# Kernel tuning notes

Measured on AMD Instinct MI355X. Metric: run time of the kernel, lower is better.

## Reference

```python
import jax, jax.numpy as jnp
import numpy as np

BATCH = 4096
NUM_INPUTS = 784
WIDTH = 16000        # neurons per logic layer, divisible by NUM_CLASSES
N_HIDDEN = 4         # width->width layers stacked for scan (plus the input layer)
NUM_CLASSES = 10


def setup_inputs() -> dict:
    key = jax.random.key(0)
    ks = jax.random.split(key, 7)
    x = jax.random.bernoulli(ks[0], 0.5, (BATCH, NUM_INPUTS))
    idx_a0 = jax.random.randint(ks[1], (WIDTH,), 0, NUM_INPUTS, dtype=jnp.int32)
    idx_b0 = jax.random.randint(ks[2], (WIDTH,), 0, NUM_INPUTS, dtype=jnp.int32)
    neg0 = jax.random.bernoulli(ks[3], 0.5, (WIDTH, 2))
    idx_a = jax.random.randint(ks[4], (N_HIDDEN, WIDTH), 0, WIDTH, dtype=jnp.int32)
    idx_b = jax.random.randint(ks[5], (N_HIDDEN, WIDTH), 0, WIDTH, dtype=jnp.int32)
    neg = jax.random.bernoulli(ks[6], 0.5, (N_HIDDEN, WIDTH, 2))
    return {"x": x, "idx_a0": idx_a0, "idx_b0": idx_b0, "neg0": neg0,
            "idx_a": idx_a, "idx_b": idx_b, "neg": neg}


def _gate(a, b, nf):
    # gate = (maybe-NOT a) AND (maybe-NOT b); NOT on booleans == XOR with flag
    return (a ^ nf[:, 0]) & (b ^ nf[:, 1])


def reference(x, idx_a0, idx_b0, neg0, idx_a, idx_b, neg):
    # input layer: gather wires from the boolean input
    h = _gate(x[:, idx_a0], x[:, idx_b0], neg0)  # [BATCH, WIDTH] bool

    def step(h, p):
        ia, ib, nf = p
        return _gate(h[:, ia], h[:, ib], nf), None

    h, _ = jax.lax.scan(step, h, (idx_a, idx_b, neg))
    # GroupSum: popcount per class group -> int32 logits
    out = h.reshape(BATCH, NUM_CLASSES, WIDTH // NUM_CLASSES).sum(-1, dtype=jnp.int32)
    return out
```

## Files before the change

### kernel.cpp

```cpp
#include <hip/hip_runtime.h>


#define NIN   784
#define WIDTH 16000
#define NH    4
#define NC    10
#define GPC   1600
#define NBLK  128
#define TPB   1024
#define SSTR  13

typedef unsigned int u32;

__global__ void desc_kernel(const int* __restrict__ ia0, const int* __restrict__ ib0,
                            const int* __restrict__ n0,
                            const int* __restrict__ ia, const int* __restrict__ ib,
                            const int* __restrict__ n, u32* __restrict__ desc) {
    int t = blockIdx.x * blockDim.x + threadIdx.x;
    if (t >= (NH + 1) * WIDTH) return;
    int l = t / WIDTH, g = t % WIDTH;
    int a, b, na, nb;
    if (l == 0) { a = ia0[g]; b = ib0[g]; na = n0[2 * g]; nb = n0[2 * g + 1]; }
    else {
        int o = (l - 1) * WIDTH + g;
        a = ia[o]; b = ib[o]; na = n[2 * o]; nb = n[2 * o + 1];
    }
    desc[t] = (u32)a | ((u32)b << 14) | (na ? (1u << 28) : 0u) | (nb ? (1u << 29) : 0u);
}

__device__ __forceinline__ void gate(const u32* __restrict__ src, u32* __restrict__ dst,
                                     const u32* __restrict__ dp, int g) {
    u32 d  = dp[g];
    u32 a  = d & 0x3FFFu;
    u32 b  = (d >> 14) & 0x3FFFu;
    u32 ma = 0u - ((d >> 28) & 1u);
    u32 mb = 0u - ((d >> 29) & 1u);
    dst[g] = (src[a] ^ ma) & (src[b] ^ mb);
}

__launch_bounds__(TPB)
__global__ void net_kernel(const int* __restrict__ x, const u32* __restrict__ desc,
                           int* __restrict__ out) {
    __shared__ u32 xw[NIN];
    __shared__ u32 bufA[WIDTH];
    __shared__ u32 bufB[WIDTH];

    int w = blockIdx.x;
    int t = threadIdx.x;

    if (t < NIN) {
        const int* base = x + (size_t)(w * 32) * NIN + t;
        u32 acc = 0;
#pragma unroll
        for (int r = 0; r < 32; ++r)
            acc |= (base[(size_t)r * NIN] != 0 ? 1u : 0u) << r;
        xw[t] = acc;
    }
    __syncthreads();

    {
        const u32* dp = desc;
#pragma unroll 3
        for (int it = 0; it < 15; ++it) gate(xw, bufA, dp, t + it * TPB);
        if (t < WIDTH - 15 * TPB) gate(xw, bufA, dp, t + 15 * TPB);
    }

    u32* cur = bufA;
    u32* nxt = bufB;
    for (int l = 1; l <= NH; ++l) {
        __syncthreads();
        const u32* dp = desc + (size_t)l * WIDTH;
#pragma unroll 3
        for (int it = 0; it < 15; ++it) gate(cur, nxt, dp, t + it * TPB);
        if (t < WIDTH - 15 * TPB) gate(cur, nxt, dp, t + 15 * TPB);
        u32* tmp = cur; cur = nxt; nxt = tmp;
    }
    __syncthreads();

    u32* scratch = nxt;
    if (t < NC * 100) {
        int c = t / 100, j = t % 100;
        u32 p[12];
#pragma unroll
        for (int q = 0; q < 12; ++q) p[q] = 0;
#pragma unroll
        for (int k = 0; k < 16; ++k) {
            u32 carry = cur[c * GPC + k * 100 + j];
#pragma unroll
            for (int q = 0; q < 5; ++q) { u32 s = p[q]; p[q] = s ^ carry; carry = s & carry; }
        }
        u32* sp = scratch + (c * 100 + j) * SSTR;
#pragma unroll
        for (int q = 0; q < 12; ++q) sp[q] = p[q];
    }

    const int widths[8] = {100, 50, 25, 13, 7, 4, 2, 1};
    for (int s = 0; s < 7; ++s) {
        int W = widths[s], Wo = widths[s + 1];
        u32 p[12];
        bool act = (t < NC * Wo);
        int c = 0, j = 0;
        __syncthreads();
        if (act) {
            c = t / Wo; j = t % Wo;
            const u32* pa = scratch + (c * 100 + 2 * j) * SSTR;
#pragma unroll
            for (int q = 0; q < 12; ++q) p[q] = pa[q];
            if (2 * j + 1 < W) {
                const u32* pb = scratch + (c * 100 + 2 * j + 1) * SSTR;
                u32 carry = 0;
#pragma unroll
                for (int q = 0; q < 12; ++q) {
                    u32 a = p[q], b = pb[q];
                    u32 xr = a ^ b;
                    p[q] = xr ^ carry;
                    carry = (a & b) | (carry & xr);
                }
            }
        }
        __syncthreads();
        if (act) {
            u32* po = scratch + (c * 100 + j) * SSTR;
#pragma unroll
            for (int q = 0; q < 12; ++q) po[q] = p[q];
        }
    }
    __syncthreads();

    if (t < NC * 32) {
        int c = t / 32, bit = t % 32;
        const u32* sp = scratch + (c * 100) * SSTR;
        int cnt = 0;
#pragma unroll
        for (int q = 0; q < 12; ++q) cnt += (int)((sp[q] >> bit) & 1u) << q;
        out[((size_t)w * 32 + bit) * NC + c] = cnt;
    }
}

extern "C" void kernel_launch(void* const* d_in, const int* in_sizes, int n_in,
                              void* d_out, int out_size, void* d_ws, size_t ws_size,
                              hipStream_t stream) {
    const int* x      = (const int*)d_in[0];
    const int* idx_a0 = (const int*)d_in[1];
    const int* idx_b0 = (const int*)d_in[2];
    const int* neg0   = (const int*)d_in[3];
    const int* idx_a  = (const int*)d_in[4];
    const int* idx_b  = (const int*)d_in[5];
    const int* neg    = (const int*)d_in[6];
    int* out = (int*)d_out;

    u32* desc = (u32*)d_ws;

    int ndesc = (NH + 1) * WIDTH;
    desc_kernel<<<(ndesc + 255) / 256, 256, 0, stream>>>(
        idx_a0, idx_b0, neg0, idx_a, idx_b, neg, desc);

    net_kernel<<<NBLK, TPB, 0, stream>>>(x, desc, out);
}
```

Baseline: 92.19 us.

## Prefetch gate descriptors into registers and batch LDS gathers per layer

Pads each layer's descriptor array to 16384 entries so every thread handles exactly 16 gates with no tail branch. Each thread keeps its descriptors in registers and prefetches the next layer's descriptors while evaluating the current layer, hiding global-load latency. LDS gathers are issued in batches of eight before the gates are computed, to raise memory-level parallelism. The trade-off is higher register pressure and a larger shared-memory footprint from the padded buffers.

```diff
diff --git a/kernel.cpp b/kernel.cpp
--- a/kernel.cpp
+++ b/kernel.cpp
@@ -3,11 +3,13 @@
 
 #define NIN   784
 #define WIDTH 16000
+#define SW    16384
 #define NH    4
 #define NC    10
 #define GPC   1600
 #define NBLK  128
 #define TPB   1024
+#define NIT   16
 #define SSTR  13
 
 typedef unsigned int u32;
@@ -17,36 +19,35 @@
                             const int* __restrict__ ia, const int* __restrict__ ib,
                             const int* __restrict__ n, u32* __restrict__ desc) {
     int t = blockIdx.x * blockDim.x + threadIdx.x;
-    if (t >= (NH + 1) * WIDTH) return;
-    int l = t / WIDTH, g = t % WIDTH;
-    int a, b, na, nb;
-    if (l == 0) { a = ia0[g]; b = ib0[g]; na = n0[2 * g]; nb = n0[2 * g + 1]; }
-    else {
-        int o = (l - 1) * WIDTH + g;
-        a = ia[o]; b = ib[o]; na = n[2 * o]; nb = n[2 * o + 1];
+    if (t >= (NH + 1) * SW) return;
+    int l = t >> 14;
+    int g = t & (SW - 1);
+    u32 d = 0;
+    if (g < WIDTH) {
+        int a, b, na, nb;
+        if (l == 0) { a = ia0[g]; b = ib0[g]; na = n0[2 * g]; nb = n0[2 * g + 1]; }
+        else {
+            int o = (l - 1) * WIDTH + g;
+            a = ia[o]; b = ib[o]; na = n[2 * o]; nb = n[2 * o + 1];
+        }
+        d = (u32)a | ((u32)b << 14) | (na ? (1u << 28) : 0u) | (nb ? (1u << 29) : 0u);
     }
-    desc[t] = (u32)a | ((u32)b << 14) | (na ? (1u << 28) : 0u) | (nb ? (1u << 29) : 0u);
-}
-
-__device__ __forceinline__ void gate(const u32* __restrict__ src, u32* __restrict__ dst,
-                                     const u32* __restrict__ dp, int g) {
-    u32 d  = dp[g];
-    u32 a  = d & 0x3FFFu;
-    u32 b  = (d >> 14) & 0x3FFFu;
-    u32 ma = 0u - ((d >> 28) & 1u);
-    u32 mb = 0u - ((d >> 29) & 1u);
-    dst[g] = (src[a] ^ ma) & (src[b] ^ mb);
+    desc[t] = d;
 }
 
 __launch_bounds__(TPB)
 __global__ void net_kernel(const int* __restrict__ x, const u32* __restrict__ desc,
                            int* __restrict__ out) {
     __shared__ u32 xw[NIN];
-    __shared__ u32 bufA[WIDTH];
-    __shared__ u32 bufB[WIDTH];
+    __shared__ u32 bufA[SW];
+    __shared__ u32 bufB[SW];
 
     int w = blockIdx.x;
     int t = threadIdx.x;
+
+    u32 dreg[NIT];
+#pragma unroll
+    for (int it = 0; it < NIT; ++it) dreg[it] = desc[t + it * TPB];
 
     if (t < NIN) {
         const int* base = x + (size_t)(w * 32) * NIN + t;
@@ -58,26 +59,42 @@
     }
     __syncthreads();
 
-    {
-        const u32* dp = desc;
-#pragma unroll 3
-        for (int it = 0; it < 15; ++it) gate(xw, bufA, dp, t + it * TPB);
-        if (t < WIDTH - 15 * TPB) gate(xw, bufA, dp, t + 15 * TPB);
+    u32* cur = xw;
+#pragma unroll
+    for (int l = 0; l <= NH; ++l) {
+        u32* dst = (l & 1) ? bufB : bufA;
+        u32 dn[NIT];
+        if (l < NH) {
+            const u32* dq = desc + (size_t)(l + 1) * SW;
+#pragma unroll
+            for (int it = 0; it < NIT; ++it) dn[it] = dq[t + it * TPB];
+        }
+#pragma unroll
+        for (int half = 0; half < 2; ++half) {
+            u32 av[8], bv[8];
+#pragma unroll
+            for (int j = 0; j < 8; ++j) {
+                u32 d = dreg[half * 8 + j];
+                av[j] = cur[d & 0x3FFFu];
+                bv[j] = cur[(d >> 14) & 0x3FFFu];
+            }
+#pragma unroll
+            for (int j = 0; j < 8; ++j) {
+                int it = half * 8 + j;
+                u32 d = dreg[it];
+                u32 ma = 0u - ((d >> 28) & 1u);
+                u32 mb = 0u - ((d >> 29) & 1u);
+                dst[t + it * TPB] = (av[j] ^ ma) & (bv[j] ^ mb);
+            }
+        }
+        __syncthreads();
+#pragma unroll
+        for (int it = 0; it < NIT; ++it) dreg[it] = dn[it];
+        cur = dst;
     }
+    u32* res = bufA;
+    u32* scratch = bufB;
 
-    u32* cur = bufA;
-    u32* nxt = bufB;
-    for (int l = 1; l <= NH; ++l) {
-        __syncthreads();
-        const u32* dp = desc + (size_t)l * WIDTH;
-#pragma unroll 3
-        for (int it = 0; it < 15; ++it) gate(cur, nxt, dp, t + it * TPB);
-        if (t < WIDTH - 15 * TPB) gate(cur, nxt, dp, t + 15 * TPB);
-        u32* tmp = cur; cur = nxt; nxt = tmp;
-    }
-    __syncthreads();
-
-    u32* scratch = nxt;
     if (t < NC * 100) {
         int c = t / 100, j = t % 100;
         u32 p[12];
@@ -85,7 +102,7 @@
         for (int q = 0; q < 12; ++q) p[q] = 0;
 #pragma unroll
         for (int k = 0; k < 16; ++k) {
-            u32 carry = cur[c * GPC + k * 100 + j];
+            u32 carry = res[c * GPC + k * 100 + j];
 #pragma unroll
             for (int q = 0; q < 5; ++q) { u32 s = p[q]; p[q] = s ^ carry; carry = s & carry; }
         }
@@ -151,7 +168,7 @@
 
     u32* desc = (u32*)d_ws;
 
-    int ndesc = (NH + 1) * WIDTH;
+    int ndesc = (NH + 1) * SW;
     desc_kernel<<<(ndesc + 255) / 256, 256, 0, stream>>>(
         idx_a0, idx_b0, neg0, idx_a, idx_b, neg, desc);
 
```

Measured after the change: 88.66 us. 3.8% less time.
